# Performance work log

Measured on AMD Instinct MI355X. Metric: run time of the kernel, lower is better.

Reference implementation:

```python
import jax, jax.numpy as jnp
import numpy as np

N, E = 25000, 400000
NIN, NOUT, HID = 32, 32, 128


def setup_inputs() -> dict:
    key = jax.random.key(0)
    ks = jax.random.split(key, 8)
    s = lambda d: 1.0 / np.sqrt(d)
    return {
        "x": jax.random.normal(ks[0], (N, NIN), jnp.float32),
        "edge_index": jax.random.randint(ks[1], (2, E), 0, N, jnp.int64),
        "edge_attr": jax.random.normal(ks[2], (E, NIN), jnp.float32),
        # edge-MLP: Linear(NIN,HID) -> ReLU -> Linear(HID, NIN*NOUT)
        "w1": jax.random.normal(ks[3], (NIN, HID), jnp.float32) * s(NIN),
        "b1": jnp.zeros((HID,), jnp.float32),
        "w2": jax.random.normal(ks[4], (HID, NIN * NOUT), jnp.float32) * s(HID),
        "b2": jnp.zeros((NIN * NOUT,), jnp.float32),
        # NNConv root weight and bias
        "root": jax.random.normal(ks[5], (NIN, NOUT), jnp.float32) * s(NIN),
        "bias": jnp.zeros((NOUT,), jnp.float32),
    }


def reference(x, edge_index, edge_attr, w1, b1, w2, b2, root, bias):
    src, dst = edge_index[0], edge_index[1]
    # per-edge weight matrices from edge-attr MLP: [E, NIN, NOUT]
    h = jax.nn.relu(edge_attr @ w1 + b1)
    W = (h @ w2 + b2).reshape(-1, NIN, NOUT)
    # gather source features, per-edge small matmul: [E, NOUT]
    msg = jnp.einsum("ei,eio->eo", x[src], W)
    # scatter-add to target nodes (PyG default aggr='add')
    agg = jax.ops.segment_sum(msg, dst, num_segments=N)
    # root/self transform + bias
    return agg + x @ root + bias
```

## Files before the change

### kernel.cpp

```cpp
#include <hip/hip_runtime.h>
#include <hip/hip_fp16.h>


#define NN 25000
#define EE 400000

typedef _Float16 f16x8 __attribute__((ext_vector_type(8)));
typedef float    f32x16 __attribute__((ext_vector_type(16)));

__global__ __launch_bounds__(256) void prep_kernel(
    const float* __restrict__ w1, const float* __restrict__ w2,
    const float* __restrict__ b2,
    _Float16* __restrict__ w2p, _Float16* __restrict__ w1p, _Float16* __restrict__ b2p,
    float4* __restrict__ part4, int nzero4)
{
    int b = blockIdx.x;
    if (b < 532) {
        int t = b * 256 + threadIdx.x;
        if (t < 131072) {
            int j = t & 7, lane = (t >> 3) & 63, ih = (t >> 9) & 1, c = t >> 10;
            w2p[t] = (_Float16)w2[c * 1024 + (ih * 16 + ((lane >> 5) << 3) + j) * 32 + (lane & 31)];
        } else if (t < 135168) {
            int u = t - 131072;
            int j = u & 7, lane = (u >> 3) & 63, kk = (u >> 9) & 1, r = u >> 10;
            w1p[u] = (_Float16)w1[(kk * 16 + ((lane >> 5) << 3) + j) * 128 + r * 32 + (lane & 31)];
        } else {
            int u = t - 135168;
            int j = u & 7, lane = (u >> 3) & 63, ih = u >> 9;
            b2p[u] = (_Float16)b2[(ih * 16 + ((lane >> 5) << 3) + j) * 32 + (lane & 31)];
        }
    } else {
        int z = (b - 532) * 256 + threadIdx.x;
        if (z < nzero4) part4[z] = make_float4(0.f, 0.f, 0.f, 0.f);
    }
}

__global__ __launch_bounds__(256) void final_kernel(
    const float* __restrict__ x, const float* __restrict__ root,
    const float* __restrict__ bias, const float* __restrict__ part,
    int ncopies, float* __restrict__ out)
{
    int gid = blockIdx.x * 256 + threadIdx.x;
    int n = gid >> 5, o = gid & 31;
    float acc = bias[o];
    const float* xr = x + (n << 5);
#pragma unroll
    for (int i = 0; i < 32; ++i)
        acc = fmaf(xr[i], root[(i << 5) + o], acc);
    for (int c = 0; c < ncopies; ++c) acc += part[(size_t)c * 800000 + gid];
    out[gid] = acc;
}

__global__ __launch_bounds__(256, 3) void edge_kernel(
    const float*    __restrict__ x,
    const int*      __restrict__ ei,
    const float*    __restrict__ ea,
    const float*    __restrict__ b1,
    const _Float16* __restrict__ w2p,
    const _Float16* __restrict__ w1p,
    const _Float16* __restrict__ b2p,
    float* __restrict__ outp, int copyMask)
{
    __shared__ unsigned short hTq[4][16][32][2];

    const int t    = threadIdx.x;
    const int w    = t >> 6;
    const int lane = t & 63;
    const int l    = lane & 31;
    const int half = lane >> 5;

    const int  ebraw = blockIdx.x * 256 + w * 64;
    const bool live  = (ebraw + 64) <= EE;
    const int  ebw   = live ? ebraw : (EE - 64);

    float* __restrict__ myout = outp + (size_t)(blockIdx.x & copyMask) * 800000;

    union u8h { f16x8 v; __half2 h2[4]; };

    const f16x8* __restrict__ w2f = (const f16x8*)w2p;

    f16x8 B0[4], B1[4];
    auto loadHalf = [&](int hc, f16x8 (&B)[4]) {
        const f16x8* p = w2f + (size_t)hc * 256 + lane;
#pragma unroll
        for (int fi = 0; fi < 4; ++fi) B[fi] = p[fi * 64];
    };
    loadHalf(0, B0);
    loadHalf(1, B1);

    u8h eaf[2][2];
#pragma unroll
    for (int g = 0; g < 2; ++g)
#pragma unroll
        for (int kk = 0; kk < 2; ++kk) {
            const float* p = ea + (ebw + g * 32 + l) * 32 + kk * 16 + half * 8;
            float4 a0 = *(const float4*)p;
            float4 a1 = *(const float4*)(p + 4);
            eaf[g][kk].h2[0] = __float22half2_rn(make_float2(a0.x, a0.y));
            eaf[g][kk].h2[1] = __float22half2_rn(make_float2(a0.z, a0.w));
            eaf[g][kk].h2[2] = __float22half2_rn(make_float2(a1.x, a1.y));
            eaf[g][kk].h2[3] = __float22half2_rn(make_float2(a1.z, a1.w));
        }

    __half2 xs0[8], xs1[8];
    {
        int s0 = ei[ebw + l], s1 = ei[ebw + 32 + l];
#pragma unroll
        for (int ih = 0; ih < 2; ++ih) {
            float4 a0 = *(const float4*)(x + s0 * 32 + ih * 16 + half * 8);
            float4 a1 = *(const float4*)(x + s0 * 32 + ih * 16 + half * 8 + 4);
            xs0[ih*4+0] = __float22half2_rn(make_float2(a0.x, a0.y));
            xs0[ih*4+1] = __float22half2_rn(make_float2(a0.z, a0.w));
            xs0[ih*4+2] = __float22half2_rn(make_float2(a1.x, a1.y));
            xs0[ih*4+3] = __float22half2_rn(make_float2(a1.z, a1.w));
            float4 c0 = *(const float4*)(x + s1 * 32 + ih * 16 + half * 8);
            float4 c1 = *(const float4*)(x + s1 * 32 + ih * 16 + half * 8 + 4);
            xs1[ih*4+0] = __float22half2_rn(make_float2(c0.x, c0.y));
            xs1[ih*4+1] = __float22half2_rn(make_float2(c0.z, c0.w));
            xs1[ih*4+2] = __float22half2_rn(make_float2(c1.x, c1.y));
            xs1[ih*4+3] = __float22half2_rn(make_float2(c1.z, c1.w));
        }
    }

    f32x16 acc0, acc1;
#pragma unroll
    for (int i = 0; i < 16; ++i) { acc0[i] = 0.f; acc1[i] = 0.f; }

    unsigned held[8];

    auto phase1 = [&](int r) {
        f16x8 w1f0 = *(const f16x8*)(w1p + ((r * 2 + 0) * 64 + lane) * 8);
        f16x8 w1f1 = *(const f16x8*)(w1p + ((r * 2 + 1) * 64 + lane) * 8);
#pragma unroll
        for (int g = 0; g < 2; ++g) {
            f32x16 h;
#pragma unroll
            for (int i = 0; i < 16; ++i) h[i] = 0.f;
            h = __builtin_amdgcn_mfma_f32_32x32x16_f16(w1f0, eaf[g][0].v, h, 0, 0, 0);
            h = __builtin_amdgcn_mfma_f32_32x32x16_f16(w1f1, eaf[g][1].v, h, 0, 0, 0);
#pragma unroll
            for (int i = 0; i < 16; ++i) {
                int row = (i & 3) + ((i >> 2) << 3) + (half << 2);
                float hv = fmaxf(h[i] + b1[r * 32 + row], 0.f);
                unsigned short us = __half_as_ushort(__float2half(hv));
                if (i < 8) {
                    hTq[w][row][l][g] = us;
                } else {
                    int j = i - 8;
                    if (g == 0) held[j] = us;
                    else        held[j] |= (unsigned)us << 16;
                }
            }
        }
    };

    auto flushHeld = [&]() {
#pragma unroll
        for (int j = 0; j < 8; ++j) {
            int slot = (j & 3) + ((j >> 2) << 3) + (half << 2);
            *(unsigned*)&hTq[w][slot][l][0] = held[j];
        }
    };

    auto computeHalf = [&](int q4, int hh, const f16x8 (&B)[4]) {
#pragma unroll
        for (int c2 = 0; c2 < 2; ++c2) {
            const int cl = hh * 2 + c2;
            unsigned u = *(const unsigned*)&hTq[w][(q4 << 2) + cl][l][0];
            __half2 hp = *reinterpret_cast<const __half2*>(&u);
            __half2 h0 = __half2half2(__low2half(hp));
            __half2 h1 = __half2half2(__high2half(hp));
#pragma unroll
            for (int ih = 0; ih < 2; ++ih) {
                f16x8 bfr = B[c2 * 2 + ih];
                u8h A;
#pragma unroll
                for (int p = 0; p < 4; ++p)
                    A.h2[p] = __hmul2(h0, xs0[ih * 4 + p]);
                acc0 = __builtin_amdgcn_mfma_f32_32x32x16_f16(A.v, bfr, acc0, 0, 0, 0);
#pragma unroll
                for (int p = 0; p < 4; ++p)
                    A.h2[p] = __hmul2(h1, xs1[ih * 4 + p]);
                acc1 = __builtin_amdgcn_mfma_f32_32x32x16_f16(A.v, bfr, acc1, 0, 0, 0);
            }
        }
    };

    phase1(0);
#pragma unroll 1
    for (int r = 0; r < 4; ++r) {
        if (r > 0) phase1(r);
#pragma unroll
        for (int q = 0; q < 8; ++q) {
            const int cc = r * 8 + q;
            if (q == 4) flushHeld();
            computeHalf(q & 3, 0, B0);
            if (cc < 31) loadHalf(cc * 2 + 2, B0);
            computeHalf(q & 3, 1, B1);
            if (cc < 31) loadHalf(cc * 2 + 3, B1);
        }
    }

#pragma unroll
    for (int ih = 0; ih < 2; ++ih) {
        f16x8 bfr = *(const f16x8*)(b2p + (ih * 64 + lane) * 8);
        u8h A;
#pragma unroll
        for (int p = 0; p < 4; ++p) A.h2[p] = xs0[ih * 4 + p];
        acc0 = __builtin_amdgcn_mfma_f32_32x32x16_f16(A.v, bfr, acc0, 0, 0, 0);
#pragma unroll
        for (int p = 0; p < 4; ++p) A.h2[p] = xs1[ih * 4 + p];
        acc1 = __builtin_amdgcn_mfma_f32_32x32x16_f16(A.v, bfr, acc1, 0, 0, 0);
    }

    if (live) {
#pragma unroll
        for (int i = 0; i < 16; ++i) {
            int el = (i & 3) + ((i >> 2) << 3) + (half << 2);
            atomicAdd(myout + ei[EE + ebw +      el] * 32 + l, acc0[i]);
            atomicAdd(myout + ei[EE + ebw + 32 + el] * 32 + l, acc1[i]);
        }
    }
}

extern "C" void kernel_launch(void* const* d_in, const int* in_sizes, int n_in,
                              void* d_out, int out_size, void* d_ws, size_t ws_size,
                              hipStream_t stream) {
    const float* x    = (const float*)d_in[0];
    const int*   ei   = (const int*)  d_in[1];
    const float* ea   = (const float*)d_in[2];
    const float* w1   = (const float*)d_in[3];
    const float* b1   = (const float*)d_in[4];
    const float* w2   = (const float*)d_in[5];
    const float* b2   = (const float*)d_in[6];
    const float* root = (const float*)d_in[7];
    const float* bias = (const float*)d_in[8];
    float* out = (float*)d_out;

    _Float16* w2p = (_Float16*)d_ws;
    _Float16* w1p = (_Float16*)((char*)d_ws + 262144);
    _Float16* b2p = (_Float16*)((char*)d_ws + 270336);
    const size_t partOff = 272384;
    const size_t one = 800000ull * sizeof(float);
    size_t avail = (ws_size > partOff) ? ws_size - partOff : 0;
    int nc = 0;
    for (int c = 8; c >= 1; c >>= 1)
        if ((size_t)c * one <= avail) { nc = c; break; }

    float* part = (float*)((char*)d_ws + partOff);
    if (nc > 0) {
        int nzero4 = nc * 200000;
        int zb = (nzero4 + 255) / 256;
        prep_kernel<<<532 + zb, 256, 0, stream>>>(w1, w2, b2, w2p, w1p, b2p,
                                                  (float4*)part, nzero4);
        edge_kernel<<<(EE + 255) / 256, 256, 0, stream>>>(x, ei, ea, b1, w2p, w1p, b2p,
                                                          part, nc - 1);
        final_kernel<<<(NN * 32) / 256, 256, 0, stream>>>(x, root, bias, part, nc, out);
    } else {
        prep_kernel<<<532, 256, 0, stream>>>(w1, w2, b2, w2p, w1p, b2p, (float4*)part, 0);
        final_kernel<<<(NN * 32) / 256, 256, 0, stream>>>(x, root, bias, part, 0, out);
        edge_kernel<<<(EE + 255) / 256, 256, 0, stream>>>(x, ei, ea, b1, w2p, w1p, b2p,
                                                          out, 0);
    }
}
```

Baseline: 227.8 us.

## Process 128 edges per wave to amortize w2 fragment loads across four groups

```diff
diff --git a/kernel.cpp b/kernel.cpp
--- a/kernel.cpp
+++ b/kernel.cpp
@@ -51,7 +51,7 @@
     out[gid] = acc;
 }
 
-__global__ __launch_bounds__(256, 3) void edge_kernel(
+__global__ __launch_bounds__(128, 3) void edge_kernel(
     const float*    __restrict__ x,
     const int*      __restrict__ ei,
     const float*    __restrict__ ea,
@@ -61,7 +61,7 @@
     const _Float16* __restrict__ b2p,
     float* __restrict__ outp, int copyMask)
 {
-    __shared__ unsigned short hTq[4][16][32][2];
+    __shared__ unsigned short hTq[2][32][32][4];
 
     const int t    = threadIdx.x;
     const int w    = t >> 6;
@@ -69,9 +69,9 @@
     const int l    = lane & 31;
     const int half = lane >> 5;
 
-    const int  ebraw = blockIdx.x * 256 + w * 64;
-    const bool live  = (ebraw + 64) <= EE;
-    const int  ebw   = live ? ebraw : (EE - 64);
+    const int  ebraw = blockIdx.x * 256 + w * 128;
+    const bool live  = (ebraw + 128) <= EE;
+    const int  ebw   = live ? ebraw : (EE - 128);
 
     float* __restrict__ myout = outp + (size_t)(blockIdx.x & copyMask) * 800000;
 
@@ -79,147 +79,127 @@
 
     const f16x8* __restrict__ w2f = (const f16x8*)w2p;
 
-    f16x8 B0[4], B1[4];
-    auto loadHalf = [&](int hc, f16x8 (&B)[4]) {
-        const f16x8* p = w2f + (size_t)hc * 256 + lane;
-#pragma unroll
-        for (int fi = 0; fi < 4; ++fi) B[fi] = p[fi * 64];
+    f16x8 BA[2], BB[2];
+    auto loadCol = [&](int j, f16x8 (&B)[2]) {
+        const f16x8* p = w2f + (size_t)j * 128 + lane;
+        B[0] = p[0];
+        B[1] = p[64];
     };
-    loadHalf(0, B0);
-    loadHalf(1, B1);
-
-    u8h eaf[2][2];
-#pragma unroll
-    for (int g = 0; g < 2; ++g)
-#pragma unroll
-        for (int kk = 0; kk < 2; ++kk) {
-            const float* p = ea + (ebw + g * 32 + l) * 32 + kk * 16 + half * 8;
-            float4 a0 = *(const float4*)p;
-            float4 a1 = *(const float4*)(p + 4);
-            eaf[g][kk].h2[0] = __float22half2_rn(make_float2(a0.x, a0.y));
-            eaf[g][kk].h2[1] = __float22half2_rn(make_float2(a0.z, a0.w));
-            eaf[g][kk].h2[2] = __float22half2_rn(make_float2(a1.x, a1.y));
-            eaf[g][kk].h2[3] = __float22half2_rn(make_float2(a1.z, a1.w));
-        }
-
-    __half2 xs0[8], xs1[8];
-    {
-        int s0 = ei[ebw + l], s1 = ei[ebw + 32 + l];
+    loadCol(0, BA);
+    loadCol(1, BB);
+
+    __half2 xs[4][8];
+#pragma unroll
+    for (int g = 0; g < 4; ++g) {
+        int s = ei[ebw + g * 32 + l];
 #pragma unroll
         for (int ih = 0; ih < 2; ++ih) {
-            float4 a0 = *(const float4*)(x + s0 * 32 + ih * 16 + half * 8);
-            float4 a1 = *(const float4*)(x + s0 * 32 + ih * 16 + half * 8 + 4);
-            xs0[ih*4+0] = __float22half2_rn(make_float2(a0.x, a0.y));
-            xs0[ih*4+1] = __float22half2_rn(make_float2(a0.z, a0.w));
-            xs0[ih*4+2] = __float22half2_rn(make_float2(a1.x, a1.y));
-            xs0[ih*4+3] = __float22half2_rn(make_float2(a1.z, a1.w));
-            float4 c0 = *(const float4*)(x + s1 * 32 + ih * 16 + half * 8);
-            float4 c1 = *(const float4*)(x + s1 * 32 + ih * 16 + half * 8 + 4);
-            xs1[ih*4+0] = __float22half2_rn(make_float2(c0.x, c0.y));
-            xs1[ih*4+1] = __float22half2_rn(make_float2(c0.z, c0.w));
-            xs1[ih*4+2] = __float22half2_rn(make_float2(c1.x, c1.y));
-            xs1[ih*4+3] = __float22half2_rn(make_float2(c1.z, c1.w));
-        }
-    }
-
-    f32x16 acc0, acc1;
-#pragma unroll
-    for (int i = 0; i < 16; ++i) { acc0[i] = 0.f; acc1[i] = 0.f; }
-
-    unsigned held[8];
+            float4 a0 = *(const float4*)(x + s * 32 + ih * 16 + half * 8);
+            float4 a1 = *(const float4*)(x + s * 32 + ih * 16 + half * 8 + 4);
+            xs[g][ih*4+0] = __float22half2_rn(make_float2(a0.x, a0.y));
+            xs[g][ih*4+1] = __float22half2_rn(make_float2(a0.z, a0.w));
+            xs[g][ih*4+2] = __float22half2_rn(make_float2(a1.x, a1.y));
+            xs[g][ih*4+3] = __float22half2_rn(make_float2(a1.z, a1.w));
+        }
+    }
+
+    f32x16 acc[4];
+#pragma unroll
+    for (int g = 0; g < 4; ++g)
+#pragma unroll
+        for (int i = 0; i < 16; ++i) acc[g][i] = 0.f;
 
     auto phase1 = [&](int r) {
         f16x8 w1f0 = *(const f16x8*)(w1p + ((r * 2 + 0) * 64 + lane) * 8);
         f16x8 w1f1 = *(const f16x8*)(w1p + ((r * 2 + 1) * 64 + lane) * 8);
 #pragma unroll
-        for (int g = 0; g < 2; ++g) {
+        for (int g = 0; g < 4; ++g) {
+            const float* p = ea + (size_t)(ebw + g * 32 + l) * 32 + half * 8;
+            u8h e0, e1;
+            {
+                float4 a0 = *(const float4*)(p);
+                float4 a1 = *(const float4*)(p + 4);
+                e0.h2[0] = __float22half2_rn(make_float2(a0.x, a0.y));
+                e0.h2[1] = __float22half2_rn(make_float2(a0.z, a0.w));
+                e0.h2[2] = __float22half2_rn(make_float2(a1.x, a1.y));
+                e0.h2[3] = __float22half2_rn(make_float2(a1.z, a1.w));
+                float4 c0 = *(const float4*)(p + 16);
+                float4 c1 = *(const float4*)(p + 20);
+                e1.h2[0] = __float22half2_rn(make_float2(c0.x, c0.y));
+                e1.h2[1] = __float22half2_rn(make_float2(c0.z, c0.w));
+                e1.h2[2] = __float22half2_rn(make_float2(c1.x, c1.y));
+                e1.h2[3] = __float22half2_rn(make_float2(c1.z, c1.w));
+            }
             f32x16 h;
 #pragma unroll
             for (int i = 0; i < 16; ++i) h[i] = 0.f;
-            h = __builtin_amdgcn_mfma_f32_32x32x16_f16(w1f0, eaf[g][0].v, h, 0, 0, 0);
-            h = __builtin_amdgcn_mfma_f32_32x32x16_f16(w1f1, eaf[g][1].v, h, 0, 0, 0);
+            h = __builtin_amdgcn_mfma_f32_32x32x16_f16(w1f0, e0.v, h, 0, 0, 0);
+            h = __builtin_amdgcn_mfma_f32_32x32x16_f16(w1f1, e1.v, h, 0, 0, 0);
 #pragma unroll
             for (int i = 0; i < 16; ++i) {
                 int row = (i & 3) + ((i >> 2) << 3) + (half << 2);
                 float hv = fmaxf(h[i] + b1[r * 32 + row], 0.f);
-                unsigned short us = __half_as_ushort(__float2half(hv));
-                if (i < 8) {
-                    hTq[w][row][l][g] = us;
-                } else {
-                    int j = i - 8;
-                    if (g == 0) held[j] = us;
-                    else        held[j] |= (unsigned)us << 16;
-                }
+                hTq[w][row][l][g] = __half_as_ushort(__float2half(hv));
             }
         }
     };
 
-    auto flushHeld = [&]() {
-#pragma unroll
-        for (int j = 0; j < 8; ++j) {
-            int slot = (j & 3) + ((j >> 2) << 3) + (half << 2);
-            *(unsigned*)&hTq[w][slot][l][0] = held[j];
+    auto computeCol = [&](int cs, const f16x8 (&B)[2]) {
+        uint2 u = *(const uint2*)&hTq[w][cs][l][0];
+        __half2 ha = *reinterpret_cast<const __half2*>(&u.x);
+        __half2 hb = *reinterpret_cast<const __half2*>(&u.y);
+        __half2 d[4];
+        d[0] = __half2half2(__low2half(ha));
+        d[1] = __half2half2(__high2half(ha));
+        d[2] = __half2half2(__low2half(hb));
+        d[3] = __half2half2(__high2half(hb));
+#pragma unroll
+        for (int ih = 0; ih < 2; ++ih) {
+            f16x8 bfr = B[ih];
+#pragma unroll
+            for (int g = 0; g < 4; ++g) {
+                u8h A;
+#pragma unroll
+                for (int p = 0; p < 4; ++p)
+                    A.h2[p] = __hmul2(d[g], xs[g][ih * 4 + p]);
+                acc[g] = __builtin_amdgcn_mfma_f32_32x32x16_f16(A.v, bfr, acc[g], 0, 0, 0);
+            }
         }
     };
 
-    auto computeHalf = [&](int q4, int hh, const f16x8 (&B)[4]) {
-#pragma unroll
-        for (int c2 = 0; c2 < 2; ++c2) {
-            const int cl = hh * 2 + c2;
-            unsigned u = *(const unsigned*)&hTq[w][(q4 << 2) + cl][l][0];
-            __half2 hp = *reinterpret_cast<const __half2*>(&u);
-            __half2 h0 = __half2half2(__low2half(hp));
-            __half2 h1 = __half2half2(__high2half(hp));
-#pragma unroll
-            for (int ih = 0; ih < 2; ++ih) {
-                f16x8 bfr = B[c2 * 2 + ih];
-                u8h A;
-#pragma unroll
-                for (int p = 0; p < 4; ++p)
-                    A.h2[p] = __hmul2(h0, xs0[ih * 4 + p]);
-                acc0 = __builtin_amdgcn_mfma_f32_32x32x16_f16(A.v, bfr, acc0, 0, 0, 0);
-#pragma unroll
-                for (int p = 0; p < 4; ++p)
-                    A.h2[p] = __hmul2(h1, xs1[ih * 4 + p]);
-                acc1 = __builtin_amdgcn_mfma_f32_32x32x16_f16(A.v, bfr, acc1, 0, 0, 0);
-            }
-        }
-    };
-
-    phase1(0);
 #pragma unroll 1
     for (int r = 0; r < 4; ++r) {
-        if (r > 0) phase1(r);
-#pragma unroll
+        phase1(r);
+#pragma unroll 1
         for (int q = 0; q < 8; ++q) {
-            const int cc = r * 8 + q;
-            if (q == 4) flushHeld();
-            computeHalf(q & 3, 0, B0);
-            if (cc < 31) loadHalf(cc * 2 + 2, B0);
-            computeHalf(q & 3, 1, B1);
-            if (cc < 31) loadHalf(cc * 2 + 3, B1);
+            const int j = r * 32 + q * 4;
+            computeCol(q * 4 + 0, BA); loadCol(j + 2, BA);
+            computeCol(q * 4 + 1, BB); loadCol(j + 3, BB);
+            computeCol(q * 4 + 2, BA); loadCol(j + 4, BA);
+            computeCol(q * 4 + 3, BB); loadCol(j + 5, BB);
         }
     }
 
 #pragma unroll
     for (int ih = 0; ih < 2; ++ih) {
         f16x8 bfr = *(const f16x8*)(b2p + (ih * 64 + lane) * 8);
-        u8h A;
-#pragma unroll
-        for (int p = 0; p < 4; ++p) A.h2[p] = xs0[ih * 4 + p];
-        acc0 = __builtin_amdgcn_mfma_f32_32x32x16_f16(A.v, bfr, acc0, 0, 0, 0);
-#pragma unroll
-        for (int p = 0; p < 4; ++p) A.h2[p] = xs1[ih * 4 + p];
-        acc1 = __builtin_amdgcn_mfma_f32_32x32x16_f16(A.v, bfr, acc1, 0, 0, 0);
+#pragma unroll
+        for (int g = 0; g < 4; ++g) {
+            u8h A;
+#pragma unroll
+            for (int p = 0; p < 4; ++p) A.h2[p] = xs[g][ih * 4 + p];
+            acc[g] = __builtin_amdgcn_mfma_f32_32x32x16_f16(A.v, bfr, acc[g], 0, 0, 0);
+        }
     }
 
     if (live) {
 #pragma unroll
-        for (int i = 0; i < 16; ++i) {
-            int el = (i & 3) + ((i >> 2) << 3) + (half << 2);
-            atomicAdd(myout + ei[EE + ebw +      el] * 32 + l, acc0[i]);
-            atomicAdd(myout + ei[EE + ebw + 32 + el] * 32 + l, acc1[i]);
-        }
+        for (int g = 0; g < 4; ++g)
+#pragma unroll
+            for (int i = 0; i < 16; ++i) {
+                int el = (i & 3) + ((i >> 2) << 3) + (half << 2);
+                atomicAdd(myout + ei[EE + ebw + g * 32 + el] * 32 + l, acc[g][i]);
+            }
     }
 }
 
@@ -253,13 +233,13 @@
         int zb = (nzero4 + 255) / 256;
         prep_kernel<<<532 + zb, 256, 0, stream>>>(w1, w2, b2, w2p, w1p, b2p,
                                                   (float4*)part, nzero4);
-        edge_kernel<<<(EE + 255) / 256, 256, 0, stream>>>(x, ei, ea, b1, w2p, w1p, b2p,
+        edge_kernel<<<(EE + 255) / 256, 128, 0, stream>>>(x, ei, ea, b1, w2p, w1p, b2p,
                                                           part, nc - 1);
         final_kernel<<<(NN * 32) / 256, 256, 0, stream>>>(x, root, bias, part, nc, out);
     } else {
         prep_kernel<<<532, 256, 0, stream>>>(w1, w2, b2, w2p, w1p, b2p, (float4*)part, 0);
         final_kernel<<<(NN * 32) / 256, 256, 0, stream>>>(x, root, bias, part, 0, out);
-        edge_kernel<<<(EE + 255) / 256, 256, 0, stream>>>(x, ei, ea, b1, w2p, w1p, b2p,
+        edge_kernel<<<(EE + 255) / 256, 128, 0, stream>>>(x, ei, ea, b1, w2p, w1p, b2p,
                                                           out, 0);
     }
 }
```

Result: slower. 302.7 us (+32.9%).

## Drop partial-copy buffers, fuse prep with root transform, deepen w2 prefetch

Applied to the files above, without the earlier changes.

```diff
diff --git a/kernel.cpp b/kernel.cpp
--- a/kernel.cpp
+++ b/kernel.cpp
@@ -8,50 +8,39 @@
 typedef _Float16 f16x8 __attribute__((ext_vector_type(8)));
 typedef float    f32x16 __attribute__((ext_vector_type(16)));
 
-__global__ __launch_bounds__(256) void prep_kernel(
+__global__ __launch_bounds__(256) void prep_final_kernel(
+    const float* __restrict__ x, const float* __restrict__ root,
+    const float* __restrict__ bias,
     const float* __restrict__ w1, const float* __restrict__ w2,
     const float* __restrict__ b2,
     _Float16* __restrict__ w2p, _Float16* __restrict__ w1p, _Float16* __restrict__ b2p,
-    float4* __restrict__ part4, int nzero4)
+    float* __restrict__ out)
 {
-    int b = blockIdx.x;
-    if (b < 532) {
-        int t = b * 256 + threadIdx.x;
-        if (t < 131072) {
-            int j = t & 7, lane = (t >> 3) & 63, ih = (t >> 9) & 1, c = t >> 10;
-            w2p[t] = (_Float16)w2[c * 1024 + (ih * 16 + ((lane >> 5) << 3) + j) * 32 + (lane & 31)];
-        } else if (t < 135168) {
-            int u = t - 131072;
-            int j = u & 7, lane = (u >> 3) & 63, kk = (u >> 9) & 1, r = u >> 10;
-            w1p[u] = (_Float16)w1[(kk * 16 + ((lane >> 5) << 3) + j) * 128 + r * 32 + (lane & 31)];
-        } else {
-            int u = t - 135168;
-            int j = u & 7, lane = (u >> 3) & 63, ih = u >> 9;
-            b2p[u] = (_Float16)b2[(ih * 16 + ((lane >> 5) << 3) + j) * 32 + (lane & 31)];
-        }
-    } else {
-        int z = (b - 532) * 256 + threadIdx.x;
-        if (z < nzero4) part4[z] = make_float4(0.f, 0.f, 0.f, 0.f);
-    }
-}
-
-__global__ __launch_bounds__(256) void final_kernel(
-    const float* __restrict__ x, const float* __restrict__ root,
-    const float* __restrict__ bias, const float* __restrict__ part,
-    int ncopies, float* __restrict__ out)
-{
-    int gid = blockIdx.x * 256 + threadIdx.x;
-    int n = gid >> 5, o = gid & 31;
+    const int t = blockIdx.x * 256 + threadIdx.x;
+
+    if (t < 131072) {
+        int j = t & 7, lane = (t >> 3) & 63, ih = (t >> 9) & 1, c = t >> 10;
+        w2p[t] = (_Float16)w2[c * 1024 + (ih * 16 + ((lane >> 5) << 3) + j) * 32 + (lane & 31)];
+    } else if (t < 135168) {
+        int u = t - 131072;
+        int j = u & 7, lane = (u >> 3) & 63, kk = (u >> 9) & 1, r = u >> 10;
+        w1p[u] = (_Float16)w1[(kk * 16 + ((lane >> 5) << 3) + j) * 128 + r * 32 + (lane & 31)];
+    } else if (t < 136192) {
+        int u = t - 135168;
+        int j = u & 7, lane = (u >> 3) & 63, ih = u >> 9;
+        b2p[u] = (_Float16)b2[(ih * 16 + ((lane >> 5) << 3) + j) * 32 + (lane & 31)];
+    }
+
+    int n = t >> 5, o = t & 31;
     float acc = bias[o];
     const float* xr = x + (n << 5);
 #pragma unroll
     for (int i = 0; i < 32; ++i)
         acc = fmaf(xr[i], root[(i << 5) + o], acc);
-    for (int c = 0; c < ncopies; ++c) acc += part[(size_t)c * 800000 + gid];
-    out[gid] = acc;
+    out[t] = acc;
 }
 
-__global__ __launch_bounds__(256, 3) void edge_kernel(
+__global__ __launch_bounds__(256, 2) void edge_kernel(
     const float*    __restrict__ x,
     const int*      __restrict__ ei,
     const float*    __restrict__ ea,
@@ -59,7 +48,7 @@
     const _Float16* __restrict__ w2p,
     const _Float16* __restrict__ w1p,
     const _Float16* __restrict__ b2p,
-    float* __restrict__ outp, int copyMask)
+    float* __restrict__ out)
 {
     __shared__ unsigned short hTq[4][16][32][2];
 
@@ -73,27 +62,27 @@
     const bool live  = (ebraw + 64) <= EE;
     const int  ebw   = live ? ebraw : (EE - 64);
 
-    float* __restrict__ myout = outp + (size_t)(blockIdx.x & copyMask) * 800000;
-
     union u8h { f16x8 v; __half2 h2[4]; };
 
     const f16x8* __restrict__ w2f = (const f16x8*)w2p;
 
-    f16x8 B0[4], B1[4];
+    f16x8 H0[4], H1[4], H2[4], H3[4];
     auto loadHalf = [&](int hc, f16x8 (&B)[4]) {
         const f16x8* p = w2f + (size_t)hc * 256 + lane;
 #pragma unroll
         for (int fi = 0; fi < 4; ++fi) B[fi] = p[fi * 64];
     };
-    loadHalf(0, B0);
-    loadHalf(1, B1);
+    loadHalf(0, H0);
+    loadHalf(1, H1);
+    loadHalf(2, H2);
+    loadHalf(3, H3);
 
     u8h eaf[2][2];
 #pragma unroll
     for (int g = 0; g < 2; ++g)
 #pragma unroll
         for (int kk = 0; kk < 2; ++kk) {
-            const float* p = ea + (ebw + g * 32 + l) * 32 + kk * 16 + half * 8;
+            const float* p = ea + (size_t)(ebw + g * 32 + l) * 32 + kk * 16 + half * 8;
             float4 a0 = *(const float4*)p;
             float4 a1 = *(const float4*)(p + 4);
             eaf[g][kk].h2[0] = __float22half2_rn(make_float2(a0.x, a0.y));
@@ -190,14 +179,18 @@
 #pragma unroll 1
     for (int r = 0; r < 4; ++r) {
         if (r > 0) phase1(r);
-#pragma unroll
+#pragma unroll 1
         for (int q = 0; q < 8; ++q) {
             const int cc = r * 8 + q;
+            const int hc = cc * 2;
             if (q == 4) flushHeld();
-            computeHalf(q & 3, 0, B0);
-            if (cc < 31) loadHalf(cc * 2 + 2, B0);
-            computeHalf(q & 3, 1, B1);
-            if (cc < 31) loadHalf(cc * 2 + 3, B1);
+            if ((hc & 2) == 0) {
+                computeHalf(q & 3, 0, H0); loadHalf(hc + 4, H0);
+                computeHalf(q & 3, 1, H1); loadHalf(hc + 5, H1);
+            } else {
+                computeHalf(q & 3, 0, H2); loadHalf(hc + 4, H2);
+                computeHalf(q & 3, 1, H3); loadHalf(hc + 5, H3);
+            }
         }
     }
 
@@ -217,8 +210,8 @@
 #pragma unroll
         for (int i = 0; i < 16; ++i) {
             int el = (i & 3) + ((i >> 2) << 3) + (half << 2);
-            atomicAdd(myout + ei[EE + ebw +      el] * 32 + l, acc0[i]);
-            atomicAdd(myout + ei[EE + ebw + 32 + el] * 32 + l, acc1[i]);
+            atomicAdd(out + (size_t)ei[EE + ebw +      el] * 32 + l, acc0[i]);
+            atomicAdd(out + (size_t)ei[EE + ebw + 32 + el] * 32 + l, acc1[i]);
         }
     }
 }
@@ -240,26 +233,10 @@
     _Float16* w2p = (_Float16*)d_ws;
     _Float16* w1p = (_Float16*)((char*)d_ws + 262144);
     _Float16* b2p = (_Float16*)((char*)d_ws + 270336);
-    const size_t partOff = 272384;
-    const size_t one = 800000ull * sizeof(float);
-    size_t avail = (ws_size > partOff) ? ws_size - partOff : 0;
-    int nc = 0;
-    for (int c = 8; c >= 1; c >>= 1)
-        if ((size_t)c * one <= avail) { nc = c; break; }
-
-    float* part = (float*)((char*)d_ws + partOff);
-    if (nc > 0) {
-        int nzero4 = nc * 200000;
-        int zb = (nzero4 + 255) / 256;
-        prep_kernel<<<532 + zb, 256, 0, stream>>>(w1, w2, b2, w2p, w1p, b2p,
-                                                  (float4*)part, nzero4);
-        edge_kernel<<<(EE + 255) / 256, 256, 0, stream>>>(x, ei, ea, b1, w2p, w1p, b2p,
-                                                          part, nc - 1);
-        final_kernel<<<(NN * 32) / 256, 256, 0, stream>>>(x, root, bias, part, nc, out);
-    } else {
-        prep_kernel<<<532, 256, 0, stream>>>(w1, w2, b2, w2p, w1p, b2p, (float4*)part, 0);
-        final_kernel<<<(NN * 32) / 256, 256, 0, stream>>>(x, root, bias, part, 0, out);
-        edge_kernel<<<(EE + 255) / 256, 256, 0, stream>>>(x, ei, ea, b1, w2p, w1p, b2p,
-                                                          out, 0);
-    }
+
+    prep_final_kernel<<<(NN * 32) / 256, 256, 0, stream>>>(
+        x, root, bias, w1, w2, b2, w2p, w1p, b2p, out);
+
+    edge_kernel<<<(EE + 255) / 256, 256, 0, stream>>>(
+        x, ei, ea, b1, w2p, w1p, b2p, out);
 }
```

Measured after the change: 241.9 us. +6.2%, slower.
